# Kernel tuning notes

Measured on AMD Instinct MI355X. Metric: run time of the kernel, lower is better.

Reference implementation:

```python
import jax, jax.numpy as jnp
import numpy as np

HEADS = 8
DHEAD = 64
KSIZE = 7


def setup_inputs() -> dict:
    key = jax.random.key(0)
    k1, k2, k3, k4 = jax.random.split(key, 4)
    b, H, W, C = 16, 56, 56, 256
    inner = HEADS * DHEAD  # 512
    x = jax.random.normal(k1, (b, H, W, C), jnp.float32)
    Wq = jax.random.normal(k2, (1, 1, C, inner), jnp.float32) * 0.02
    Wkv = jax.random.normal(k3, (KSIZE, KSIZE, C, 2 * inner), jnp.float32) * 0.02
    Wo = jax.random.normal(k4, (1, 1, inner, C), jnp.float32) * 0.02
    bo = jnp.zeros((C,), jnp.float32)
    return {"x": x, "Wq": Wq, "Wkv": Wkv, "Wo": Wo, "bo": bo}


def reference(x, Wq, Wkv, Wo, bo):
    heads, dh = HEADS, DHEAD
    scale = dh ** -0.5
    b, H, W, C = x.shape
    # 1x1 conv Q projection == per-pixel matmul
    q = jnp.einsum('bhwc,cf->bhwf', x, Wq[0, 0])  # [b,H,W,inner]
    # k x k strided conv KV downsample (SAME==VALID since H%k==0)
    kv = jax.lax.conv_general_dilated(
        x, Wkv, window_strides=(KSIZE, KSIZE), padding='VALID',
        dimension_numbers=('NHWC', 'HWIO', 'NHWC'))  # [b,H/k,W/k,2*inner]
    k_, v_ = jnp.split(kv, 2, axis=-1)

    def split_heads(t):
        B, hh, ww, _ = t.shape
        return t.reshape(B, hh * ww, heads, dh)  # [b, seq, h, d]

    q = split_heads(q)      # [b, H*W, h, d]
    k_ = split_heads(k_)    # [b, (H/k)*(W/k), h, d]
    v_ = split_heads(v_)
    dots = jnp.einsum('bqhd,bkhd->bhqk', q, k_) * scale
    attn = jax.nn.softmax(dots, axis=-1)
    out = jnp.einsum('bhqk,bkhd->bqhd', attn, v_)
    out = out.reshape(b, H, W, heads * dh)
    # output 1x1 conv with bias (dropout rate 0 -> identity)
    out = jnp.einsum('bhwf,fc->bhwc', out, Wo[0, 0]) + bo
    return out
```

## Files before the change

### kernel.cpp

```cpp
#include <hip/hip_runtime.h>
#include <stdint.h>

typedef unsigned short ushort_t;
typedef __attribute__((ext_vector_type(8))) unsigned short ushort8v;
typedef __attribute__((ext_vector_type(8))) short short8v;
typedef __attribute__((ext_vector_type(4))) float f32x4;

__device__ __forceinline__ float bf2f(ushort_t u) {
  union { unsigned int i; float f; } v;
  v.i = ((unsigned int)u) << 16;
  return v.f;
}
__device__ __forceinline__ ushort_t f2bf(float f) {
  union { float f; unsigned int i; } v;
  v.f = f;
  unsigned int r = v.i + 0x7FFFu + ((v.i >> 16) & 1u);
  return (ushort_t)(r >> 16);
}

__device__ __forceinline__ ushort8v load8bf(const ushort_t* __restrict__ p) {
  return *(const ushort8v*)p;
}
__device__ __forceinline__ ushort8v load8bf(const float* __restrict__ p) {
  const float4 a = *(const float4*)p;
  const float4 b = *(const float4*)(p + 4);
  ushort8v r;
  r[0] = f2bf(a.x); r[1] = f2bf(a.y); r[2] = f2bf(a.z); r[3] = f2bf(a.w);
  r[4] = f2bf(b.x); r[5] = f2bf(b.y); r[6] = f2bf(b.z); r[7] = f2bf(b.w);
  return r;
}
__device__ __forceinline__ void storeC(float* p, float v) { *p = v; }
__device__ __forceinline__ void storeC(ushort_t* p, float v) { *p = f2bf(v); }

__global__ __launch_bounds__(256) void transpose_cvt(
    const float* __restrict__ W, ushort_t* __restrict__ WT, int K, int N) {
  __shared__ float tile[32][33];
  const int t = threadIdx.x;
  const int k0 = blockIdx.y * 32;
  const int n0 = blockIdx.x * 32;
  {
    const int r = t >> 3, c4 = (t & 7) * 4;
    const float4 v = *(const float4*)(W + (size_t)(k0 + r) * N + n0 + c4);
    tile[r][c4] = v.x; tile[r][c4 + 1] = v.y;
    tile[r][c4 + 2] = v.z; tile[r][c4 + 3] = v.w;
  }
  __syncthreads();
  {
    const int rn = t >> 3, ck = (t & 7) * 4;
    union { ushort_t u[4]; uint2 v; } o;
#pragma unroll
    for (int j = 0; j < 4; ++j) o.u[j] = f2bf(tile[ck + j][rn]);
    *(uint2*)(WT + (size_t)(n0 + rn) * K + k0 + ck) = o.v;
  }
}

__global__ __launch_bounds__(256) void cvt_f32_bf16(
    const float* __restrict__ in, ushort_t* __restrict__ out) {
  const int i = (blockIdx.x * 256 + threadIdx.x) * 4;
  const float4 v = *(const float4*)(in + i);
  union { ushort_t u[4]; uint2 q; } o;
  o.u[0] = f2bf(v.x); o.u[1] = f2bf(v.y);
  o.u[2] = f2bf(v.z); o.u[3] = f2bf(v.w);
  *(uint2*)(out + i) = o.q;
}

template <typename TA, typename TC>
__global__ __launch_bounds__(256) void gemm_mfma_nt(
    const TA* __restrict__ A, const ushort_t* __restrict__ BT,
    const float* __restrict__ bias, TC* __restrict__ C,
    int M, int N, int K, int has_bias) {
  __shared__ ushort_t lA[8 * 512];
  __shared__ ushort_t lB[8 * 512];
  const int t = threadIdx.x;
  const int m0 = blockIdx.y * 128;
  const int n0 = blockIdx.x * 128;
  const int lane = t & 63;
  const int wm = (t >> 6) >> 1, wn = (t >> 6) & 1;

  f32x4 acc[4][4] = {};

  const int sm = t >> 2;
  const int kq = t & 3;

  for (int k0 = 0; k0 < K; k0 += 32) {
#pragma unroll
    for (int h = 0; h < 2; ++h) {
      const int m = h * 64 + sm;
      const int off = (m >> 4) * 512 + (kq * 16 + (m & 15)) * 8;
      const ushort8v av = load8bf(A + (size_t)(m0 + m) * K + k0 + kq * 8);
      *(ushort8v*)&lA[off] = av;
      const ushort8v bv = load8bf(BT + (size_t)(n0 + m) * K + k0 + kq * 8);
      *(ushort8v*)&lB[off] = bv;
    }
    __syncthreads();
    short8v af[4], bf[4];
#pragma unroll
    for (int i = 0; i < 4; ++i) {
      af[i] = *(const short8v*)&lA[(wm * 4 + i) * 512 + lane * 8];
      bf[i] = *(const short8v*)&lB[(wn * 4 + i) * 512 + lane * 8];
    }
#pragma unroll
    for (int i = 0; i < 4; ++i)
#pragma unroll
      for (int j = 0; j < 4; ++j)
        acc[i][j] = __builtin_amdgcn_mfma_f32_16x16x32_bf16(
            af[i], bf[j], acc[i][j], 0, 0, 0);
    __syncthreads();
  }

  const int col = lane & 15, rq = (lane >> 4) * 4;
#pragma unroll
  for (int i = 0; i < 4; ++i) {
    const int mb = m0 + (wm * 4 + i) * 16 + rq;
#pragma unroll
    for (int j = 0; j < 4; ++j) {
      const int nb = n0 + (wn * 4 + j) * 16 + col;
      const float badd = has_bias ? bias[nb] : 0.f;
#pragma unroll
      for (int r = 0; r < 4; ++r)
        storeC(&C[(size_t)(mb + r) * N + nb], acc[i][j][r] + badd);
    }
  }
}

template <typename TA>
__global__ __launch_bounds__(256) void gemm_kv_mfma(
    const TA* __restrict__ x, const ushort_t* __restrict__ WkvT,
    float* __restrict__ C) {
  __shared__ ushort_t lA[8 * 512];
  __shared__ ushort_t lB[8 * 512];
  const int t = threadIdx.x;
  const int bl = blockIdx.x;
  const int m0 = (bl & 7) * 128;
  const int n0 = ((bl >> 3) & 7) * 128;
  const int kbeg = (bl >> 6) * 896;
  const int lane = t & 63;
  const int wm = (t >> 6) >> 1, wn = (t >> 6) & 1;

  f32x4 acc[4][4] = {};

  const int sm = t >> 2;
  const int kq = t & 3;

  for (int k0 = kbeg; k0 < kbeg + 896; k0 += 32) {
#pragma unroll
    for (int h = 0; h < 2; ++h) {
      const int m = h * 64 + sm;
      const int off = (m >> 4) * 512 + (kq * 16 + (m & 15)) * 8;
      const int gm = m0 + m;
      const int b = gm >> 6, ty = (gm >> 3) & 7, tx = gm & 7;
      const int k = k0 + kq * 8;
      const int patch = k >> 8;
      const int c = k & 255;
      const int dy = (patch * 37) >> 8;
      const int dx = patch - dy * 7;
      const int pix = b * 3136 + (ty * 7 + dy) * 56 + (tx * 7 + dx);
      const ushort8v av = load8bf(x + (size_t)pix * 256 + c);
      *(ushort8v*)&lA[off] = av;
      const ushort8v bv =
          load8bf(WkvT + (size_t)(n0 + m) * 12544 + k0 + kq * 8);
      *(ushort8v*)&lB[off] = bv;
    }
    __syncthreads();
    short8v af[4], bf[4];
#pragma unroll
    for (int i = 0; i < 4; ++i) {
      af[i] = *(const short8v*)&lA[(wm * 4 + i) * 512 + lane * 8];
      bf[i] = *(const short8v*)&lB[(wn * 4 + i) * 512 + lane * 8];
    }
#pragma unroll
    for (int i = 0; i < 4; ++i)
#pragma unroll
      for (int j = 0; j < 4; ++j)
        acc[i][j] = __builtin_amdgcn_mfma_f32_16x16x32_bf16(
            af[i], bf[j], acc[i][j], 0, 0, 0);
    __syncthreads();
  }

  const int col = lane & 15, rq = (lane >> 4) * 4;
#pragma unroll
  for (int i = 0; i < 4; ++i) {
    const int mb = m0 + (wm * 4 + i) * 16 + rq;
#pragma unroll
    for (int j = 0; j < 4; ++j) {
      const int nb = n0 + (wn * 4 + j) * 16 + col;
#pragma unroll
      for (int r = 0; r < 4; ++r)
        atomicAdd(&C[(size_t)(mb + r) * 1024 + nb], acc[i][j][r]);
    }
  }
}

__global__ __launch_bounds__(256) void attn_mfma(
    ushort_t* __restrict__ qo, const ushort_t* __restrict__ kvb) {
  __shared__ ushort_t VT[64][72];
  __shared__ ushort_t P[4][64][72];
  const int t = threadIdx.x;
  const int lane = t & 63;
  const int w = t >> 6;
  const int bh = blockIdx.y;
  const int b = bh >> 3, h = bh & 7;
  const ushort_t* kvp = kvb + (size_t)(b * 64) * 1024 + h * 64;

  for (int i = t; i < 512; i += 256) {
    const int key = i >> 3, d0 = (i & 7) * 8;
    const ushort8v v = *(const ushort8v*)(kvp + (size_t)key * 1024 + 512 + d0);
#pragma unroll
    for (int jj = 0; jj < 8; ++jj) VT[d0 + jj][key] = v[jj];
  }
  __syncthreads();

  const int q0_raw = blockIdx.x * 256 + w * 64;
  const bool valid = q0_raw < 3136;
  const int q0 = valid ? q0_raw : 3072;
  const size_t qbase = ((size_t)b * 3136 + q0) * 512 + h * 64;

  const int lm = lane & 15, quad = lane >> 4;

  short8v qf[4][2], kf[4][2];
#pragma unroll
  for (int i = 0; i < 4; ++i)
#pragma unroll
    for (int s = 0; s < 2; ++s) {
      qf[i][s] = *(const short8v*)(qo + qbase + (size_t)(16 * i + lm) * 512 +
                                   32 * s + quad * 8);
      kf[i][s] = *(const short8v*)(kvp + (size_t)(16 * i + lm) * 1024 +
                                   32 * s + quad * 8);
    }

  f32x4 sa[4][4];
#pragma unroll
  for (int i = 0; i < 4; ++i)
#pragma unroll
    for (int j = 0; j < 4; ++j) {
      f32x4 z = {};
      z = __builtin_amdgcn_mfma_f32_16x16x32_bf16(qf[i][0], kf[j][0], z, 0, 0, 0);
      sa[i][j] = __builtin_amdgcn_mfma_f32_16x16x32_bf16(qf[i][1], kf[j][1], z, 0, 0, 0);
    }

  float l[4][4];
#pragma unroll
  for (int i = 0; i < 4; ++i)
#pragma unroll
    for (int r = 0; r < 4; ++r) {
      float m = fmaxf(fmaxf(sa[i][0][r], sa[i][1][r]),
                      fmaxf(sa[i][2][r], sa[i][3][r]));
#pragma unroll
      for (int off = 1; off < 16; off <<= 1) m = fmaxf(m, __shfl_xor(m, off));
      float sum = 0.f;
#pragma unroll
      for (int j = 0; j < 4; ++j) {
        const float p = __expf(0.125f * (sa[i][j][r] - m));
        sa[i][j][r] = p;
        sum += p;
      }
#pragma unroll
      for (int off = 1; off < 16; off <<= 1) sum += __shfl_xor(sum, off);
      l[i][r] = sum;
    }

#pragma unroll
  for (int i = 0; i < 4; ++i) {
    const int row = 16 * i + quad * 4;
#pragma unroll
    for (int j = 0; j < 4; ++j) {
      const int col = 16 * j + lm;
#pragma unroll
      for (int r = 0; r < 4; ++r) P[w][row + r][col] = f2bf(sa[i][j][r]);
    }
  }
  __syncthreads();

  short8v vf[4][2];
#pragma unroll
  for (int jn = 0; jn < 4; ++jn)
#pragma unroll
    for (int s2 = 0; s2 < 2; ++s2)
      vf[jn][s2] = *(const short8v*)&VT[16 * jn + lm][32 * s2 + quad * 8];

  f32x4 oa[4][4];
#pragma unroll
  for (int i = 0; i < 4; ++i) {
    const short8v pf0 = *(const short8v*)&P[w][16 * i + lm][quad * 8];
    const short8v pf1 = *(const short8v*)&P[w][16 * i + lm][32 + quad * 8];
#pragma unroll
    for (int jn = 0; jn < 4; ++jn) {
      f32x4 z = {};
      z = __builtin_amdgcn_mfma_f32_16x16x32_bf16(pf0, vf[jn][0], z, 0, 0, 0);
      oa[i][jn] = __builtin_amdgcn_mfma_f32_16x16x32_bf16(pf1, vf[jn][1], z, 0, 0, 0);
    }
  }

  if (valid) {
#pragma unroll
    for (int i = 0; i < 4; ++i) {
#pragma unroll
      for (int r = 0; r < 4; ++r) {
        const float inv = 1.f / l[i][r];
        const size_t rowoff = qbase + (size_t)(16 * i + quad * 4 + r) * 512;
#pragma unroll
        for (int jn = 0; jn < 4; ++jn)
          qo[rowoff + 16 * jn + lm] = f2bf(oa[i][jn][r] * inv);
      }
    }
  }
}

extern "C" void kernel_launch(void* const* d_in, const int* in_sizes, int n_in,
                              void* d_out, int out_size, void* d_ws,
                              size_t ws_size, hipStream_t stream) {
  const float* x = (const float*)d_in[0];
  const float* Wq = (const float*)d_in[1];
  const float* Wkv = (const float*)d_in[2];
  const float* Wo = (const float*)d_in[3];
  const float* bo = (const float*)d_in[4];
  float* out = (float*)d_out;

  char* ws = (char*)d_ws;
  ushort_t* qbuf = (ushort_t*)(ws);
  float* kvbuf = (float*)(ws + 51380224);
  ushort_t* WkvT = (ushort_t*)(ws + 55574528);
  ushort_t* WqT = (ushort_t*)(ws + 81264640);
  ushort_t* WoT = (ushort_t*)(ws + 81526784);
  ushort_t* kvbf = (ushort_t*)(ws + 81788928);
  ushort_t* xbf = (ushort_t*)(ws + 83886080);
  const bool use_xbf = ws_size >= 109576192u;

  hipLaunchKernelGGL(transpose_cvt, dim3(16, 8), dim3(256), 0, stream, Wq, WqT,
                     256, 512);
  hipLaunchKernelGGL(transpose_cvt, dim3(32, 392), dim3(256), 0, stream, Wkv,
                     WkvT, 12544, 1024);
  hipLaunchKernelGGL(transpose_cvt, dim3(8, 16), dim3(256), 0, stream, Wo, WoT,
                     512, 256);
  hipMemsetAsync(kvbuf, 0, 1024 * 1024 * 4, stream);

  if (use_xbf) {
    hipLaunchKernelGGL(cvt_f32_bf16, dim3(12544), dim3(256), 0, stream, x,
                       xbf);
    hipLaunchKernelGGL((gemm_mfma_nt<ushort_t, ushort_t>), dim3(4, 392),
                       dim3(256), 0, stream, xbf, WqT, (const float*)nullptr,
                       qbuf, 50176, 512, 256, 0);
    hipLaunchKernelGGL((gemm_kv_mfma<ushort_t>), dim3(896), dim3(256), 0,
                       stream, xbf, WkvT, kvbuf);
  } else {
    hipLaunchKernelGGL((gemm_mfma_nt<float, ushort_t>), dim3(4, 392),
                       dim3(256), 0, stream, x, WqT, (const float*)nullptr,
                       qbuf, 50176, 512, 256, 0);
    hipLaunchKernelGGL((gemm_kv_mfma<float>), dim3(896), dim3(256), 0, stream,
                       x, WkvT, kvbuf);
  }
  hipLaunchKernelGGL(cvt_f32_bf16, dim3(1024), dim3(256), 0, stream, kvbuf,
                     kvbf);
  hipLaunchKernelGGL(attn_mfma, dim3(13, 128), dim3(256), 0, stream, qbuf,
                     kvbf);
  hipLaunchKernelGGL((gemm_mfma_nt<ushort_t, float>), dim3(2, 392), dim3(256),
                     0, stream, qbuf, WoT, bo, out, 50176, 256, 512, 1);
}
```

Baseline: 367.6 us.

## Use direct global-to-LDS loads and patch-major im2col layout for projection GEMMs

The input is now converted to bf16 straight into a patch-major (im2col) layout, so each 7x7 KV patch is contiguous along K. A new shared GEMM body loads tiles with global_load_lds (direct global-to-LDS 16-byte loads), skipping the register staging step. The Q projection reads the permuted layout through index arithmetic, and the KV GEMM uses split-K with atomic adds. This trades extra per-row div/mod address math and a different LDS access pattern for less load-path overhead and contiguous KV reads.

```diff
diff --git a/kernel.cpp b/kernel.cpp
--- a/kernel.cpp
+++ b/kernel.cpp
@@ -31,6 +31,21 @@
 }
 __device__ __forceinline__ void storeC(float* p, float v) { *p = v; }
 __device__ __forceinline__ void storeC(ushort_t* p, float v) { *p = f2bf(v); }
+
+__device__ __forceinline__ void gl16(const ushort_t* g, ushort_t* l) {
+  __builtin_amdgcn_global_load_lds(
+      (const __attribute__((address_space(1))) void*)g,
+      (__attribute__((address_space(3))) void*)l, 16, 0, 0);
+}
+
+__device__ __forceinline__ size_t pp_off(unsigned g) {
+  const unsigned b = g / 3136u;
+  const unsigned r = g - b * 3136u;
+  const unsigned y = r / 56u, xx = r - y * 56u;
+  const unsigned ty = y / 7u, dy = y - ty * 7u;
+  const unsigned tx = xx / 7u, dx = xx - tx * 7u;
+  return ((size_t)((b * 64u + ty * 8u + tx) * 49u + dy * 7u + dx)) << 8;
+}
 
 __global__ __launch_bounds__(256) void transpose_cvt(
     const float* __restrict__ W, ushort_t* __restrict__ WT, int K, int N) {
@@ -62,6 +77,120 @@
   o.u[0] = f2bf(v.x); o.u[1] = f2bf(v.y);
   o.u[2] = f2bf(v.z); o.u[3] = f2bf(v.w);
   *(uint2*)(out + i) = o.q;
+}
+
+__global__ __launch_bounds__(256) void cvt_im2col(
+    const float* __restrict__ x, ushort_t* __restrict__ xp) {
+  const int e = (blockIdx.x * 256 + threadIdx.x) * 8;
+  const unsigned p = ((unsigned)e) >> 8;
+  const int c = e & 255;
+  const float4 a = *(const float4*)(x + e);
+  const float4 b = *(const float4*)(x + e + 4);
+  ushort8v o;
+  o[0] = f2bf(a.x); o[1] = f2bf(a.y); o[2] = f2bf(a.z); o[3] = f2bf(a.w);
+  o[4] = f2bf(b.x); o[5] = f2bf(b.y); o[6] = f2bf(b.z); o[7] = f2bf(b.w);
+  *(ushort8v*)(xp + pp_off(p) + c) = o;
+}
+
+template <int MODE, bool PERMA>
+__device__ __forceinline__ void gemm_body(
+    const ushort_t* __restrict__ A, const ushort_t* __restrict__ BT,
+    const float* __restrict__ bias, void* __restrict__ Cv,
+    int N, int K, int m0, int n0, int kbeg, int kend) {
+  __shared__ ushort_t lA[8 * 512];
+  __shared__ ushort_t lB[8 * 512];
+  const int t = threadIdx.x;
+  const int lane = t & 63;
+  const int wv = __builtin_amdgcn_readfirstlane(t >> 6);
+  const int wm = wv >> 1, wn = wv & 1;
+  const int rl = lane & 15;
+  const int kof = (lane >> 4) * 8;
+
+  const ushort_t* aS[2];
+  const ushort_t* bS[2];
+  ushort_t* aD[2];
+  ushort_t* bD[2];
+#pragma unroll
+  for (int h = 0; h < 2; ++h) {
+    const int row = h * 64 + wv * 16 + rl;
+    size_t aoff;
+    if (PERMA)
+      aoff = pp_off((unsigned)(m0 + row));
+    else
+      aoff = (size_t)(m0 + row) * K;
+    aS[h] = A + aoff + kof;
+    bS[h] = BT + (size_t)(n0 + row) * K + kof;
+    aD[h] = &lA[h * 2048 + wv * 512];
+    bD[h] = &lB[h * 2048 + wv * 512];
+  }
+
+  f32x4 acc[4][4] = {};
+
+  for (int k0 = kbeg; k0 < kend; k0 += 32) {
+#pragma unroll
+    for (int h = 0; h < 2; ++h) {
+      gl16(aS[h] + k0, aD[h]);
+      gl16(bS[h] + k0, bD[h]);
+    }
+    __syncthreads();
+    short8v af[4], bfr[4];
+#pragma unroll
+    for (int i = 0; i < 4; ++i) {
+      af[i] = *(const short8v*)&lA[(wm * 4 + i) * 512 + lane * 8];
+      bfr[i] = *(const short8v*)&lB[(wn * 4 + i) * 512 + lane * 8];
+    }
+#pragma unroll
+    for (int i = 0; i < 4; ++i)
+#pragma unroll
+      for (int j = 0; j < 4; ++j)
+        acc[i][j] = __builtin_amdgcn_mfma_f32_16x16x32_bf16(
+            af[i], bfr[j], acc[i][j], 0, 0, 0);
+    __syncthreads();
+  }
+
+  const int col = lane & 15, rq = (lane >> 4) * 4;
+#pragma unroll
+  for (int i = 0; i < 4; ++i) {
+    const int mb = m0 + (wm * 4 + i) * 16 + rq;
+#pragma unroll
+    for (int j = 0; j < 4; ++j) {
+      const int nb = n0 + (wn * 4 + j) * 16 + col;
+      if (MODE == 0) {
+        ushort_t* C = (ushort_t*)Cv;
+#pragma unroll
+        for (int r = 0; r < 4; ++r)
+          C[(size_t)(mb + r) * N + nb] = f2bf(acc[i][j][r]);
+      } else if (MODE == 1) {
+        float* C = (float*)Cv;
+        const float badd = bias[nb];
+#pragma unroll
+        for (int r = 0; r < 4; ++r)
+          C[(size_t)(mb + r) * N + nb] = acc[i][j][r] + badd;
+      } else {
+        float* C = (float*)Cv;
+#pragma unroll
+        for (int r = 0; r < 4; ++r)
+          atomicAdd(&C[(size_t)(mb + r) * N + nb], acc[i][j][r]);
+      }
+    }
+  }
+}
+
+template <int MODE, bool PERMA>
+__global__ __launch_bounds__(256) void gemm_nt_2d(
+    const ushort_t* __restrict__ A, const ushort_t* __restrict__ BT,
+    const float* __restrict__ bias, void* __restrict__ C, int N, int K) {
+  gemm_body<MODE, PERMA>(A, BT, bias, C, N, K, blockIdx.y * 128,
+                         blockIdx.x * 128, 0, K);
+}
+
+__global__ __launch_bounds__(256) void gemm_kv_gl(
+    const ushort_t* __restrict__ xpat, const ushort_t* __restrict__ WkvT,
+    float* __restrict__ C) {
+  const int bl = blockIdx.x;
+  const int kbeg = (bl >> 6) * 896;
+  gemm_body<2, false>(xpat, WkvT, (const float*)nullptr, C, 1024, 12544,
+                      (bl & 7) * 128, ((bl >> 3) & 7) * 128, kbeg, kbeg + 896);
 }
 
 template <typename TA, typename TC>
@@ -323,8 +452,8 @@
   ushort_t* WqT = (ushort_t*)(ws + 81264640);
   ushort_t* WoT = (ushort_t*)(ws + 81526784);
   ushort_t* kvbf = (ushort_t*)(ws + 81788928);
-  ushort_t* xbf = (ushort_t*)(ws + 83886080);
-  const bool use_xbf = ws_size >= 109576192u;
+  ushort_t* xpat = (ushort_t*)(ws + 83886080);
+  const bool use_fast = ws_size >= 109576192u;
 
   hipLaunchKernelGGL(transpose_cvt, dim3(16, 8), dim3(256), 0, stream, Wq, WqT,
                      256, 512);
@@ -334,25 +463,31 @@
                      512, 256);
   hipMemsetAsync(kvbuf, 0, 1024 * 1024 * 4, stream);
 
-  if (use_xbf) {
-    hipLaunchKernelGGL(cvt_f32_bf16, dim3(12544), dim3(256), 0, stream, x,
-                       xbf);
-    hipLaunchKernelGGL((gemm_mfma_nt<ushort_t, ushort_t>), dim3(4, 392),
-                       dim3(256), 0, stream, xbf, WqT, (const float*)nullptr,
-                       qbuf, 50176, 512, 256, 0);
-    hipLaunchKernelGGL((gemm_kv_mfma<ushort_t>), dim3(896), dim3(256), 0,
-                       stream, xbf, WkvT, kvbuf);
+  if (use_fast) {
+    hipLaunchKernelGGL(cvt_im2col, dim3(6272), dim3(256), 0, stream, x, xpat);
+    hipLaunchKernelGGL((gemm_nt_2d<0, true>), dim3(4, 392), dim3(256), 0,
+                       stream, xpat, WqT, (const float*)nullptr, qbuf, 512,
+                       256);
+    hipLaunchKernelGGL(gemm_kv_gl, dim3(896), dim3(256), 0, stream, xpat,
+                       WkvT, kvbuf);
+    hipLaunchKernelGGL(cvt_f32_bf16, dim3(1024), dim3(256), 0, stream, kvbuf,
+                       kvbf);
+    hipLaunchKernelGGL(attn_mfma, dim3(13, 128), dim3(256), 0, stream, qbuf,
+                       kvbf);
+    hipLaunchKernelGGL((gemm_nt_2d<1, false>), dim3(2, 392), dim3(256), 0,
+                       stream, qbuf, WoT, bo, out, 256, 512);
   } else {
     hipLaunchKernelGGL((gemm_mfma_nt<float, ushort_t>), dim3(4, 392),
                        dim3(256), 0, stream, x, WqT, (const float*)nullptr,
                        qbuf, 50176, 512, 256, 0);
     hipLaunchKernelGGL((gemm_kv_mfma<float>), dim3(896), dim3(256), 0, stream,
                        x, WkvT, kvbuf);
-  }
-  hipLaunchKernelGGL(cvt_f32_bf16, dim3(1024), dim3(256), 0, stream, kvbuf,
-                     kvbf);
-  hipLaunchKernelGGL(attn_mfma, dim3(13, 128), dim3(256), 0, stream, qbuf,
-                     kvbf);
-  hipLaunchKernelGGL((gemm_mfma_nt<ushort_t, float>), dim3(2, 392), dim3(256),
-                     0, stream, qbuf, WoT, bo, out, 50176, 256, 512, 1);
-}
+    hipLaunchKernelGGL(cvt_f32_bf16, dim3(1024), dim3(256), 0, stream, kvbuf,
+                       kvbf);
+    hipLaunchKernelGGL(attn_mfma, dim3(13, 128), dim3(256), 0, stream, qbuf,
+                       kvbf);
+    hipLaunchKernelGGL((gemm_mfma_nt<ushort_t, float>), dim3(2, 392),
+                       dim3(256), 0, stream, qbuf, WoT, bo, out, 50176, 256,
+                       512, 1);
+  }
+}
```

Measured after the change: 389.7 us. +6.0%, slower.
